# Performance work log

Hardware: AMD Instinct MI355X
Metric: run time of the kernel (lower is better)

Reference implementation:

```python
import jax, jax.numpy as jnp
import numpy as np

NEG_BIG = -1.0e9


def setup_inputs() -> dict:
    key = jax.random.key(0)
    kq, kk, kv, km = jax.random.split(key, 4)
    B, Lq, Lk, D = 16, 2048, 2048, 128
    queries = jax.random.normal(kq, (B, Lq, D), dtype=jnp.float32)
    keys = jax.random.normal(kk, (B, Lk, D), dtype=jnp.float32)
    values = jax.random.normal(kv, (B, Lk, D), dtype=jnp.float32)
    mask = (jax.random.uniform(km, (Lk,)) > 0.8).astype(jnp.float32)
    return {"queries": queries, "keys": keys, "values": values, "mask": mask}


def reference(queries, keys, values, mask):
    d = keys.shape[-1]
    # scores: [B, Lq, Lk]
    scores = jnp.einsum("bqd,bkd->bqk", queries, keys) / jnp.sqrt(jnp.float32(d))
    masked = scores + mask[None, None, :] * NEG_BIG
    attn = jax.nn.softmax(masked, axis=-1)
    # dropout is identity in eval / p=0.0
    return jnp.einsum("bqk,bkd->bqd", attn, values)
```

## Files before the change

### kernel.cpp

```cpp
#include <hip/hip_runtime.h>
#include <hip/hip_bf16.h>


#define B_    16
#define LQ_   2048
#define LK_   2048
#define DIM_  128
#define NTH   256
#define SCALE_ 0.08838834764831845f
#define LOG2E_ 1.4426950408889634f
#define SC2_   (SCALE_ * LOG2E_)
#define NEGBIG -1.0e9f
#define PS 72

typedef __attribute__((ext_vector_type(8))) short bf16x8;
typedef __attribute__((ext_vector_type(4))) float f32x4;

#define GLDS(gsrc, ldst) \
  __builtin_amdgcn_global_load_lds( \
      (const __attribute__((address_space(1))) unsigned int*)(gsrc), \
      (__attribute__((address_space(3))) unsigned int*)(ldst), 16, 0, 0)

static __device__ __forceinline__ unsigned short f2bf(float f) {
    unsigned int u = __builtin_bit_cast(unsigned int, f);
    u += 0x7fff + ((u >> 16) & 1);
    return (unsigned short)(u >> 16);
}

__global__ __launch_bounds__(256) void build_idx(const float* __restrict__ Mk,
                                                 int* __restrict__ hdr,
                                                 int* __restrict__ idx)
{
    __shared__ int sc[256];
    int t = threadIdx.x;
    int keep[8], loc[8];
    int c = 0;
    #pragma unroll
    for (int j = 0; j < 8; ++j) {
        keep[j] = (Mk[t * 8 + j] < 0.5f) ? 1 : 0;
        loc[j] = c;
        c += keep[j];
    }
    sc[t] = c;
    __syncthreads();
    for (int off = 1; off < 256; off <<= 1) {
        int v = (t >= off) ? sc[t - off] : 0;
        __syncthreads();
        sc[t] += v;
        __syncthreads();
    }
    int base = sc[t] - c;
    #pragma unroll
    for (int j = 0; j < 8; ++j)
        if (keep[j]) idx[base + loc[j]] = t * 8 + j;
    if (t == 255) hdr[0] = sc[255];
}

__global__ __launch_bounds__(NTH) void pack_kv(
    const float* __restrict__ K, const float* __restrict__ V,
    const int* __restrict__ hdr, const int* __restrict__ idx,
    unsigned short* __restrict__ Kb, unsigned short* __restrict__ Vtb)
{
    const int cnt = hdr[0];
    int bid = blockIdx.x;
    if (bid < 2048) {
        int gid = bid * NTH + threadIdx.x;
        int c  = gid & 15;
        int r2 = (gid >> 4) & 63;
        int T  = gid >> 10;
        int slot = (r2 & 32) + 2 * (r2 & 15) + ((r2 >> 4) & 1);
        int j = (T & 31) * 64 + slot;
        int key = (j < cnt) ? idx[j] : 0;
        const float4* s4 = (const float4*)(K + ((size_t)(T >> 5) * LK_ + key) * DIM_ + c * 8);
        float4 a = s4[0], bq = s4[1];
        bf16x8 h = { (short)f2bf(a.x),  (short)f2bf(a.y),  (short)f2bf(a.z),  (short)f2bf(a.w),
                     (short)f2bf(bq.x), (short)f2bf(bq.y), (short)f2bf(bq.z), (short)f2bf(bq.w) };
        *(bf16x8*)(Kb + (size_t)T * 8192 + r2 * 128 + ((c ^ (r2 & 15)) * 8)) = h;
    } else {
        int T = bid - 2048;
        int w4 = threadIdx.x >> 6, lane = threadIdx.x & 63;
        const float* vb = V + (size_t)(T >> 5) * LK_ * DIM_;
        const int* ix = idx + (T & 31) * 64;
        int jbase = (T & 31) * 64;
        unsigned short* db = Vtb + (size_t)T * 8192;
        #pragma unroll
        for (int half = 0; half < 2; ++half) {
            int d = half * 64 + lane;
            #pragma unroll
            for (int cb = 0; cb < 8; cb += 4) {
                int c = cb + w4;
                float v[8];
                #pragma unroll
                for (int kk = 0; kk < 8; ++kk) {
                    int j = c * 8 + kk;
                    int key = (jbase + j < cnt) ? ix[j] : 0;
                    v[kk] = vb[(size_t)key * DIM_ + d];
                }
                bf16x8 h = { (short)f2bf(v[0]), (short)f2bf(v[1]), (short)f2bf(v[2]), (short)f2bf(v[3]),
                             (short)f2bf(v[4]), (short)f2bf(v[5]), (short)f2bf(v[6]), (short)f2bf(v[7]) };
                *(bf16x8*)(db + (c >> 2) * 4096 + d * 32 + (c & 3) * 8) = h;
            }
        }
    }
}

__global__ __launch_bounds__(NTH, 2) void attn_mfma6(
    const float* __restrict__ Q, const unsigned short* __restrict__ Kb,
    const unsigned short* __restrict__ Vtb, const int* __restrict__ hdr,
    float* __restrict__ O)
{
    __shared__ __align__(16) unsigned short sKa[8192];
    __shared__ __align__(16) unsigned short sKb_[8192];
    __shared__ __align__(16) unsigned short sP[64 * PS];
    __shared__ float sLp[64];

    const int tid  = threadIdx.x;
    const int w    = tid >> 6, lane = tid & 63;
    const int quad = lane >> 4, l15 = lane & 15;
    const int rg   = (w & 1) * 32;
    const int wh   = w >> 1;
    const int kh   = wh * 32;

    const int bid = blockIdx.x;
    const int grp = bid >> 3;
    const int b   = (bid & 7) + 8 * (grp & 1);
    const int q0  = (grp >> 1) * 64;

    const int cnt = hdr[0];
    const int nIter2 = (((cnt + 63) >> 6) + 1) & ~1;

    bf16x8 vone;
    #pragma unroll
    for (int j = 0; j < 8; ++j) vone[j] = (short)0x3F80;

    const int voff = wh * 4096 + l15 * 32 + quad * 8;

    bf16x8 aQ[2][4];
    {
        const float4* Qg = (const float4*)(Q + ((size_t)b * LQ_ + q0) * DIM_);
        #pragma unroll
        for (int h = 0; h < 2; ++h) {
            #pragma unroll
            for (int it = 0; it < 4; ++it) {
                int i2 = tid + it * NTH;
                int r = i2 >> 5, c4 = i2 & 31;
                float4 v = Qg[(h * 32 + r) * 32 + c4];
                ushort4 hh = { f2bf(v.x * SC2_), f2bf(v.y * SC2_),
                               f2bf(v.z * SC2_), f2bf(v.w * SC2_) };
                *(ushort4*)&sP[r * 128 + (((c4 >> 1) ^ (r & 15)) * 8) + (c4 & 1) * 4] = hh;
            }
            __syncthreads();
            if ((rg >> 5) == h) {
                #pragma unroll
                for (int rs = 0; rs < 2; ++rs)
                    #pragma unroll
                    for (int ks = 0; ks < 4; ++ks)
                        aQ[rs][ks] = *(const bf16x8*)&sP[(rs * 16 + l15) * 128 +
                                                         (((ks * 4 + quad) ^ l15) * 8)];
            }
            __syncthreads();
        }
    }

    {
        const char* ksrc = (const char*)Kb + (size_t)(b * 32) * 16384;
        #pragma unroll
        for (int j = 0; j < 4; ++j) {
            int o = (j * 4 + w) * 1024;
            GLDS(ksrc + o + lane * 16, (char*)sKa + o);
        }
    }
    __syncthreads();

    f32x4 acc[2][8], lacc[2];
    #pragma unroll
    for (int rs = 0; rs < 2; ++rs) {
        lacc[rs] = (f32x4){0.f, 0.f, 0.f, 0.f};
        #pragma unroll
        for (int dt = 0; dt < 8; ++dt) acc[rs][dt] = (f32x4){0.f, 0.f, 0.f, 0.f};
    }

#define TILE_BODY(CURK, NXTK, I) do {                                          \
         \
    const unsigned short* vsrc = Vtb + (size_t)(b * 32 + (I)) * 8192 + voff;   \
    bf16x8 bv[8];                                                              \
    _Pragma("unroll")                                                          \
    for (int dt = 0; dt < 8; ++dt) bv[dt] = *(const bf16x8*)(vsrc + dt * 512); \
    const int nxt = (I) + 1;                                                   \
    if (nxt < nIter2) {                                                        \
        const char* ksrc = (const char*)Kb + (size_t)(b * 32 + nxt) * 16384;   \
        _Pragma("unroll")                                                      \
        for (int j = 0; j < 4; ++j) {                                          \
            int o = (j * 4 + w) * 1024;                                        \
            GLDS(ksrc + o + lane * 16, (char*)(NXTK) + o);                     \
        }                                                                      \
    }                                                                          \
    f32x4 s_[2][2];                                                            \
    _Pragma("unroll")                                                          \
    for (int kt2 = 0; kt2 < 2; ++kt2) {                                        \
        f32x4 c0 = (f32x4){0.f,0.f,0.f,0.f}, c1 = (f32x4){0.f,0.f,0.f,0.f};   \
        _Pragma("unroll")                                                      \
        for (int ks = 0; ks < 4; ++ks) {                                       \
            bf16x8 bk = *(const bf16x8*)&(CURK)[(kh + kt2 * 16 + l15) * 128 +  \
                                                (((ks * 4 + quad) ^ l15) * 8)];\
            c0 = __builtin_amdgcn_mfma_f32_16x16x32_bf16(aQ[0][ks], bk, c0, 0,0,0); \
            c1 = __builtin_amdgcn_mfma_f32_16x16x32_bf16(aQ[1][ks], bk, c1, 0,0,0); \
        }                                                                      \
        int slot = (I) * 64 + kh + 2 * l15 + kt2;                              \
        bool kept = slot < cnt;                                                \
        _Pragma("unroll")                                                      \
        for (int r = 0; r < 4; ++r) {                                          \
            s_[0][kt2][r] = kept ? c0[r] : -1.0e30f;                           \
            s_[1][kt2][r] = kept ? c1[r] : -1.0e30f;                           \
        }                                                                      \
    }                                                                          \
    _Pragma("unroll")                                                          \
    for (int rs = 0; rs < 2; ++rs)                                             \
        _Pragma("unroll")                                                      \
        for (int r = 0; r < 4; ++r) {                                          \
            float p0 = __builtin_amdgcn_exp2f(s_[rs][0][r]);                   \
            float p1 = __builtin_amdgcn_exp2f(s_[rs][1][r]);                   \
            int row = rg + rs * 16 + quad * 4 + r;                             \
            unsigned pk = __builtin_amdgcn_perm(                               \
                __builtin_bit_cast(unsigned, p1),                              \
                __builtin_bit_cast(unsigned, p0), 0x07060302u);                \
            *(unsigned*)&sP[row * PS + kh + 2 * l15] = pk;                     \
        }                                                                      \
    {                                                                          \
        bf16x8 aP0 = *(const bf16x8*)&sP[(rg + l15) * PS + kh + quad * 8];     \
        bf16x8 aP1 = *(const bf16x8*)&sP[(rg + 16 + l15) * PS + kh + quad * 8];\
        lacc[0] = __builtin_amdgcn_mfma_f32_16x16x32_bf16(aP0, vone, lacc[0], 0,0,0); \
        lacc[1] = __builtin_amdgcn_mfma_f32_16x16x32_bf16(aP1, vone, lacc[1], 0,0,0); \
        _Pragma("unroll")                                                      \
        for (int dt = 0; dt < 8; ++dt) {                                       \
            acc[0][dt] = __builtin_amdgcn_mfma_f32_16x16x32_bf16(aP0, bv[dt], acc[0][dt], 0,0,0); \
            acc[1][dt] = __builtin_amdgcn_mfma_f32_16x16x32_bf16(aP1, bv[dt], acc[1][dt], 0,0,0); \
        }                                                                      \
    }                                                                          \
    __syncthreads();                                                           \
} while (0)

    for (int kk = 0; kk < nIter2; kk += 2) {
        TILE_BODY(sKa,  sKb_, kk);
        TILE_BODY(sKb_, sKa,  kk + 1);
    }
#undef TILE_BODY

    float* sOw = (rg == 0) ? (float*)sKa : (float*)sKb_;
    if (wh == 1) {
        #pragma unroll
        for (int rs = 0; rs < 2; ++rs)
            #pragma unroll
            for (int r = 0; r < 4; ++r) {
                int lrow = rs * 16 + quad * 4 + r;
                #pragma unroll
                for (int dt = 0; dt < 8; ++dt)
                    sOw[lrow * 128 + dt * 16 + l15] = acc[rs][dt][r];
                if (l15 == 0) sLp[rg + lrow] = lacc[rs][r];
            }
    }
    __syncthreads();
    if (wh == 0) {
        float* Og = O + ((size_t)b * LQ_ + q0 + rg) * DIM_;
        #pragma unroll
        for (int rs = 0; rs < 2; ++rs)
            #pragma unroll
            for (int r = 0; r < 4; ++r) {
                int lrow = rs * 16 + quad * 4 + r;
                float inv = 1.0f / (lacc[rs][r] + sLp[rg + lrow]);
                #pragma unroll
                for (int dt = 0; dt < 8; ++dt)
                    Og[(size_t)lrow * DIM_ + dt * 16 + l15] =
                        (acc[rs][dt][r] + sOw[lrow * 128 + dt * 16 + l15]) * inv;
            }
    }
}

#define QS 136
#define VS 72
__global__ __launch_bounds__(NTH, 2) void attn_fallback(
    const float* __restrict__ Q, const float* __restrict__ K,
    const float* __restrict__ V, const float* __restrict__ Mk,
    float* __restrict__ O)
{
    __shared__ __align__(16) unsigned short sQ[64][QS];
    __shared__ __align__(16) unsigned short sK[64][QS];
    __shared__ __align__(16) unsigned short sVt[DIM_][VS];
    __shared__ __align__(16) unsigned short sPf[64][VS];
    __shared__ float sB[64];

    const int tid  = threadIdx.x;
    const int w    = tid >> 6, lane = tid & 63;
    const int quad = lane >> 4, l15 = lane & 15;
    const int bid = blockIdx.x;
    const int grp = bid >> 3;
    const int b   = (bid & 7) + 8 * (grp & 1);
    const int q0  = (grp >> 1) * 64;

    {
        const float4* Qg = (const float4*)(Q + ((size_t)b * LQ_ + q0) * DIM_);
        #pragma unroll
        for (int it = 0; it < 8; ++it) {
            int i = tid + it * NTH;
            int r = i >> 5, c4 = i & 31;
            float4 v = Qg[r * 32 + c4];
            ushort4 h = { f2bf(v.x), f2bf(v.y), f2bf(v.z), f2bf(v.w) };
            *(ushort4*)&sQ[r][c4 * 4] = h;
        }
    }
    __syncthreads();
    bf16x8 aQ[4];
    #pragma unroll
    for (int ks = 0; ks < 4; ++ks)
        aQ[ks] = *(const bf16x8*)&sQ[w * 16 + l15][ks * 32 + quad * 8];

    float m_i[4], l_i[4];
    f32x4 acc[8];
    #pragma unroll
    for (int r = 0; r < 4; ++r) { m_i[r] = -3.0e38f; l_i[r] = 0.f; }
    #pragma unroll
    for (int dt = 0; dt < 8; ++dt) acc[dt] = (f32x4){0.f, 0.f, 0.f, 0.f};

    for (int k0 = 0; k0 < LK_; k0 += 64) {
        const float4* Kg = (const float4*)(K + ((size_t)b * LK_ + k0) * DIM_);
        const float4* Vg = (const float4*)(V + ((size_t)b * LK_ + k0) * DIM_);
        #pragma unroll
        for (int it = 0; it < 8; ++it) {
            int i = tid + it * NTH;
            int r = i >> 5, c4 = i & 31;
            float4 kv = Kg[r * 32 + c4];
            ushort4 h = { f2bf(kv.x), f2bf(kv.y), f2bf(kv.z), f2bf(kv.w) };
            *(ushort4*)&sK[r][c4 * 4] = h;
            float4 vv = Vg[r * 32 + c4];
            int d = c4 * 4;
            sVt[d + 0][r] = f2bf(vv.x);
            sVt[d + 1][r] = f2bf(vv.y);
            sVt[d + 2][r] = f2bf(vv.z);
            sVt[d + 3][r] = f2bf(vv.w);
        }
        if (tid < 64) sB[tid] = Mk[k0 + tid] * NEGBIG;
        __syncthreads();

        f32x4 s[4];
        #pragma unroll
        for (int kt = 0; kt < 4; ++kt) {
            f32x4 c = (f32x4){0.f, 0.f, 0.f, 0.f};
            #pragma unroll
            for (int ks = 0; ks < 4; ++ks) {
                bf16x8 bk = *(const bf16x8*)&sK[kt * 16 + l15][ks * 32 + quad * 8];
                c = __builtin_amdgcn_mfma_f32_16x16x32_bf16(aQ[ks], bk, c, 0, 0, 0);
            }
            float bias = sB[kt * 16 + l15];
            #pragma unroll
            for (int r = 0; r < 4; ++r) s[kt][r] = c[r] * SCALE_ + bias;
        }
        #pragma unroll
        for (int r = 0; r < 4; ++r) {
            float mx = fmaxf(fmaxf(s[0][r], s[1][r]), fmaxf(s[2][r], s[3][r]));
            #pragma unroll
            for (int off = 1; off < 16; off <<= 1) mx = fmaxf(mx, __shfl_xor(mx, off));
            float mn = fmaxf(m_i[r], mx);
            float al = __expf(m_i[r] - mn);
            m_i[r] = mn;
            float rsum = 0.f;
            #pragma unroll
            for (int kt = 0; kt < 4; ++kt) {
                float p = __expf(s[kt][r] - mn);
                rsum += p;
                sPf[w * 16 + quad * 4 + r][kt * 16 + l15] = f2bf(p);
            }
            #pragma unroll
            for (int off = 1; off < 16; off <<= 1) rsum += __shfl_xor(rsum, off);
            l_i[r] = l_i[r] * al + rsum;
            #pragma unroll
            for (int dt = 0; dt < 8; ++dt) acc[dt][r] *= al;
        }
        bf16x8 aP0 = *(const bf16x8*)&sPf[w * 16 + l15][quad * 8];
        bf16x8 aP1 = *(const bf16x8*)&sPf[w * 16 + l15][32 + quad * 8];
        #pragma unroll
        for (int dt = 0; dt < 8; ++dt) {
            bf16x8 bv0 = *(const bf16x8*)&sVt[dt * 16 + l15][quad * 8];
            bf16x8 bv1 = *(const bf16x8*)&sVt[dt * 16 + l15][32 + quad * 8];
            acc[dt] = __builtin_amdgcn_mfma_f32_16x16x32_bf16(aP0, bv0, acc[dt], 0, 0, 0);
            acc[dt] = __builtin_amdgcn_mfma_f32_16x16x32_bf16(aP1, bv1, acc[dt], 0, 0, 0);
        }
        __syncthreads();
    }
    float* Og = O + ((size_t)b * LQ_ + q0 + w * 16) * DIM_;
    #pragma unroll
    for (int r = 0; r < 4; ++r) {
        float inv = 1.0f / l_i[r];
        int row = quad * 4 + r;
        #pragma unroll
        for (int dt = 0; dt < 8; ++dt)
            Og[(size_t)row * DIM_ + dt * 16 + l15] = acc[dt][r] * inv;
    }
}

extern "C" void kernel_launch(void* const* d_in, const int* in_sizes, int n_in,
                              void* d_out, int out_size, void* d_ws, size_t ws_size,
                              hipStream_t stream)
{
    const float* Q  = (const float*)d_in[0];
    const float* K  = (const float*)d_in[1];
    const float* V  = (const float*)d_in[2];
    const float* Mk = (const float*)d_in[3];
    float* O = (float*)d_out;

    const size_t seg  = (size_t)B_ * LK_ * DIM_ * 2;
    const size_t need = 16384 + 2 * seg;
    if (ws_size >= need) {
        int* hdr = (int*)d_ws;
        int* idx = hdr + 16;
        unsigned short* Kb  = (unsigned short*)((char*)d_ws + 16384);
        unsigned short* Vtb = Kb + seg / 2;
        hipLaunchKernelGGL(build_idx, dim3(1),    dim3(256), 0, stream, Mk, hdr, idx);
        hipLaunchKernelGGL(pack_kv,   dim3(2560), dim3(NTH), 0, stream, K, V, hdr, idx, Kb, Vtb);
        hipLaunchKernelGGL(attn_mfma6, dim3(512), dim3(NTH), 0, stream, Q, Kb, Vtb, hdr, O);
    } else {
        hipLaunchKernelGGL(attn_fallback, dim3(512), dim3(NTH), 0, stream, Q, K, V, Mk, O);
    }
}
```

Measured before the change: 144.2 us.

## Software-pipeline QK of next tile with PV of current tile, prefetch K two ahead

Restructures the attention main loop so each iteration first does softmax and P·V for tile I while computing Q·K for tile I+1. K tiles are prefetched two steps ahead into the double buffer. A prologue and epilogue handle the first QK and the last PV. The first K tile load is also moved before the Q conversion so it overlaps that work, and s_setprio raises wave priority around the MFMA block. The aim is to hide LDS and exp latency behind matrix work, at the cost of more live registers and a small risk of spills or lower occupancy.

```diff
diff --git a/kernel.cpp b/kernel.cpp
--- a/kernel.cpp
+++ b/kernel.cpp
@@ -20,6 +20,8 @@
   __builtin_amdgcn_global_load_lds( \
       (const __attribute__((address_space(1))) unsigned int*)(gsrc), \
       (__attribute__((address_space(3))) unsigned int*)(ldst), 16, 0, 0)
+
+#define MFMA16(A, Bv, C) __builtin_amdgcn_mfma_f32_16x16x32_bf16((A), (Bv), (C), 0, 0, 0)
 
 static __device__ __forceinline__ unsigned short f2bf(float f) {
     unsigned int u = __builtin_bit_cast(unsigned int, f);
@@ -127,13 +129,21 @@
     const int q0  = (grp >> 1) * 64;
 
     const int cnt = hdr[0];
-    const int nIter2 = (((cnt + 63) >> 6) + 1) & ~1;
+    const int n = (((cnt + 63) >> 6) + 1) & ~1;
 
     bf16x8 vone;
     #pragma unroll
     for (int j = 0; j < 8; ++j) vone[j] = (short)0x3F80;
 
     const int voff = wh * 4096 + l15 * 32 + quad * 8;
+
+    const char* kbase = (const char*)Kb + (size_t)(b * 32) * 16384;
+
+    #pragma unroll
+    for (int j = 0; j < 4; ++j) {
+        int o = (j * 4 + w) * 1024;
+        GLDS(kbase + o + lane * 16, (char*)sKa + o);
+    }
 
     bf16x8 aQ[2][4];
     {
@@ -162,16 +172,6 @@
         }
     }
 
-    {
-        const char* ksrc = (const char*)Kb + (size_t)(b * 32) * 16384;
-        #pragma unroll
-        for (int j = 0; j < 4; ++j) {
-            int o = (j * 4 + w) * 1024;
-            GLDS(ksrc + o + lane * 16, (char*)sKa + o);
-        }
-    }
-    __syncthreads();
-
     f32x4 acc[2][8], lacc[2];
     #pragma unroll
     for (int rs = 0; rs < 2; ++rs) {
@@ -180,40 +180,35 @@
         for (int dt = 0; dt < 8; ++dt) acc[rs][dt] = (f32x4){0.f, 0.f, 0.f, 0.f};
     }
 
-#define TILE_BODY(CURK, NXTK, I) do {                                          \
-         \
-    const unsigned short* vsrc = Vtb + (size_t)(b * 32 + (I)) * 8192 + voff;   \
-    bf16x8 bv[8];                                                              \
+    f32x4 s_[2][2];
+
+#define QK_TILE(RD, TI) do {                                                   \
+    f32x4 c00 = (f32x4){0.f,0.f,0.f,0.f};                                      \
+    f32x4 c01 = (f32x4){0.f,0.f,0.f,0.f};                                      \
+    f32x4 c10 = (f32x4){0.f,0.f,0.f,0.f};                                      \
+    f32x4 c11 = (f32x4){0.f,0.f,0.f,0.f};                                      \
     _Pragma("unroll")                                                          \
-    for (int dt = 0; dt < 8; ++dt) bv[dt] = *(const bf16x8*)(vsrc + dt * 512); \
-    const int nxt = (I) + 1;                                                   \
-    if (nxt < nIter2) {                                                        \
-        const char* ksrc = (const char*)Kb + (size_t)(b * 32 + nxt) * 16384;   \
-        _Pragma("unroll")                                                      \
-        for (int j = 0; j < 4; ++j) {                                          \
-            int o = (j * 4 + w) * 1024;                                        \
-            GLDS(ksrc + o + lane * 16, (char*)(NXTK) + o);                     \
-        }                                                                      \
+    for (int ks = 0; ks < 4; ++ks) {                                           \
+        int co = ((ks * 4 + quad) ^ l15) * 8;                                  \
+        bf16x8 bk0 = *(const bf16x8*)&(RD)[(kh + l15) * 128 + co];             \
+        bf16x8 bk1 = *(const bf16x8*)&(RD)[(kh + 16 + l15) * 128 + co];        \
+        c00 = MFMA16(aQ[0][ks], bk0, c00);                                     \
+        c10 = MFMA16(aQ[1][ks], bk0, c10);                                     \
+        c01 = MFMA16(aQ[0][ks], bk1, c01);                                     \
+        c11 = MFMA16(aQ[1][ks], bk1, c11);                                     \
     }                                                                          \
-    f32x4 s_[2][2];                                                            \
+    int slot0 = (TI) * 64 + kh + 2 * l15;                                      \
+    bool k0m = slot0 < cnt, k1m = (slot0 + 1) < cnt;                           \
     _Pragma("unroll")                                                          \
-    for (int kt2 = 0; kt2 < 2; ++kt2) {                                        \
-        f32x4 c0 = (f32x4){0.f,0.f,0.f,0.f}, c1 = (f32x4){0.f,0.f,0.f,0.f};   \
-        _Pragma("unroll")                                                      \
-        for (int ks = 0; ks < 4; ++ks) {                                       \
-            bf16x8 bk = *(const bf16x8*)&(CURK)[(kh + kt2 * 16 + l15) * 128 +  \
-                                                (((ks * 4 + quad) ^ l15) * 8)];\
-            c0 = __builtin_amdgcn_mfma_f32_16x16x32_bf16(aQ[0][ks], bk, c0, 0,0,0); \
-            c1 = __builtin_amdgcn_mfma_f32_16x16x32_bf16(aQ[1][ks], bk, c1, 0,0,0); \
-        }                                                                      \
-        int slot = (I) * 64 + kh + 2 * l15 + kt2;                              \
-        bool kept = slot < cnt;                                                \
-        _Pragma("unroll")                                                      \
-        for (int r = 0; r < 4; ++r) {                                          \
-            s_[0][kt2][r] = kept ? c0[r] : -1.0e30f;                           \
-            s_[1][kt2][r] = kept ? c1[r] : -1.0e30f;                           \
-        }                                                                      \
+    for (int r = 0; r < 4; ++r) {                                              \
+        s_[0][0][r] = k0m ? c00[r] : -1.0e30f;                                 \
+        s_[0][1][r] = k1m ? c01[r] : -1.0e30f;                                 \
+        s_[1][0][r] = k0m ? c10[r] : -1.0e30f;                                 \
+        s_[1][1][r] = k1m ? c11[r] : -1.0e30f;                                 \
     }                                                                          \
+} while (0)
+
+#define SOFTMAX_AP() do {                                                      \
     _Pragma("unroll")                                                          \
     for (int rs = 0; rs < 2; ++rs)                                             \
         _Pragma("unroll")                                                      \
@@ -226,25 +221,76 @@
                 __builtin_bit_cast(unsigned, p0), 0x07060302u);                \
             *(unsigned*)&sP[row * PS + kh + 2 * l15] = pk;                     \
         }                                                                      \
+    aP0 = *(const bf16x8*)&sP[(rg + l15) * PS + kh + quad * 8];                \
+    aP1 = *(const bf16x8*)&sP[(rg + 16 + l15) * PS + kh + quad * 8];           \
+} while (0)
+
+#define BODY(RD, WR, I) do {                                                   \
+    __syncthreads();            \
     {                                                                          \
-        bf16x8 aP0 = *(const bf16x8*)&sP[(rg + l15) * PS + kh + quad * 8];     \
-        bf16x8 aP1 = *(const bf16x8*)&sP[(rg + 16 + l15) * PS + kh + quad * 8];\
-        lacc[0] = __builtin_amdgcn_mfma_f32_16x16x32_bf16(aP0, vone, lacc[0], 0,0,0); \
-        lacc[1] = __builtin_amdgcn_mfma_f32_16x16x32_bf16(aP1, vone, lacc[1], 0,0,0); \
+        int t2 = (I) + 2; if (t2 > n - 1) t2 = n - 1;                          \
+        const char* ksrc = kbase + (size_t)t2 * 16384;                         \
         _Pragma("unroll")                                                      \
-        for (int dt = 0; dt < 8; ++dt) {                                       \
-            acc[0][dt] = __builtin_amdgcn_mfma_f32_16x16x32_bf16(aP0, bv[dt], acc[0][dt], 0,0,0); \
-            acc[1][dt] = __builtin_amdgcn_mfma_f32_16x16x32_bf16(aP1, bv[dt], acc[1][dt], 0,0,0); \
+        for (int j = 0; j < 4; ++j) {                                          \
+            int o = (j * 4 + w) * 1024;                                        \
+            GLDS(ksrc + o + lane * 16, (char*)(WR) + o);                       \
         }                                                                      \
     }                                                                          \
-    __syncthreads();                                                           \
+    const unsigned short* vsrc = Vtb + (size_t)(b * 32 + (I)) * 8192 + voff;   \
+    bf16x8 bv[8];                                                              \
+    _Pragma("unroll")                                                          \
+    for (int dt = 0; dt < 8; ++dt) bv[dt] = *(const bf16x8*)(vsrc + dt * 512); \
+    bf16x8 aP0, aP1;                                                           \
+    SOFTMAX_AP();                                                              \
+    __builtin_amdgcn_s_setprio(1);                                             \
+    QK_TILE(RD, (I) + 1);          \
+    lacc[0] = MFMA16(aP0, vone, lacc[0]);                                      \
+    lacc[1] = MFMA16(aP1, vone, lacc[1]);                                      \
+    _Pragma("unroll")                                                          \
+    for (int dt = 0; dt < 8; ++dt) {                                           \
+        acc[0][dt] = MFMA16(aP0, bv[dt], acc[0][dt]);                          \
+        acc[1][dt] = MFMA16(aP1, bv[dt], acc[1][dt]);                          \
+    }                                                                          \
+    __builtin_amdgcn_s_setprio(0);                                             \
 } while (0)
 
-    for (int kk = 0; kk < nIter2; kk += 2) {
-        TILE_BODY(sKa,  sKb_, kk);
-        TILE_BODY(sKb_, sKa,  kk + 1);
-    }
-#undef TILE_BODY
+    {
+        const char* ksrc = kbase + 16384;
+        #pragma unroll
+        for (int j = 0; j < 4; ++j) {
+            int o = (j * 4 + w) * 1024;
+            GLDS(ksrc + o + lane * 16, (char*)sKb_ + o);
+        }
+    }
+    QK_TILE(sKa, 0);
+
+    int i = 0;
+    for (; i + 1 < n - 1; i += 2) {
+        BODY(sKb_, sKa, i);
+        BODY(sKa, sKb_, i + 1);
+    }
+    if (i < n - 1) BODY(sKb_, sKa, i);
+
+    {
+        const unsigned short* vsrc = Vtb + (size_t)(b * 32 + (n - 1)) * 8192 + voff;
+        bf16x8 bv[8];
+        #pragma unroll
+        for (int dt = 0; dt < 8; ++dt) bv[dt] = *(const bf16x8*)(vsrc + dt * 512);
+        bf16x8 aP0, aP1;
+        SOFTMAX_AP();
+        lacc[0] = MFMA16(aP0, vone, lacc[0]);
+        lacc[1] = MFMA16(aP1, vone, lacc[1]);
+        #pragma unroll
+        for (int dt = 0; dt < 8; ++dt) {
+            acc[0][dt] = MFMA16(aP0, bv[dt], acc[0][dt]);
+            acc[1][dt] = MFMA16(aP1, bv[dt], acc[1][dt]);
+        }
+    }
+#undef BODY
+#undef SOFTMAX_AP
+#undef QK_TILE
+
+    __syncthreads();
 
     float* sOw = (rg == 0) ? (float*)sKa : (float*)sKb_;
     if (wh == 1) {
```

Result: no change. 145.3 us (+0.8%).
